# Performance work log

Measured on AMD Instinct MI355X. Metric: run time of the kernel, lower is better.

## Reference

```python
import jax, jax.numpy as jnp
import numpy as np

LN_EPS = 1e-5


def setup_inputs() -> dict:
    key = jax.random.key(0)
    k1, k2, k3, k4 = jax.random.split(key, 4)
    b, n, d, o, m = 64, 196, 768, 196, 2
    return {
        "x": jax.random.normal(k1, (b, n, d), dtype=jnp.float32),
        "ln_w": jnp.ones((d,), dtype=jnp.float32),
        "ln_b": jnp.zeros((d,), dtype=jnp.float32),
        "sw": jax.random.normal(k2, (o, m, n), dtype=jnp.float32),
        "sb": jax.random.normal(k3, (o, m, n), dtype=jnp.float32),
        "dw": jax.random.normal(k4, (o, m), dtype=jnp.float32),
    }


def reference(x, ln_w, ln_b, sw, sb, dw):
    # LayerNorm over last dim (dim=768)
    mu = jnp.mean(x, axis=-1, keepdims=True)
    var = jnp.mean(jnp.square(x - mu), axis=-1, keepdims=True)
    y = (x - mu) * jax.lax.rsqrt(var + LN_EPS) * ln_w + ln_b  # (b, n, d)

    # Original: repeat y to (b,d,o,m,n), apply sw*y+sb, sum over n.
    # With no synapse activation / dropout this is exactly a contraction:
    # s[b,d,o,m] = sum_n sw[o,m,n]*y[b,n,d] + sum_n sb[o,m,n]
    s = jnp.einsum('bnd,omn->bdom', y, sw) + jnp.sum(sb, axis=-1)  # (b,d,o,m)

    # dendritic weighting then sum over branches m
    t = jnp.sum(dw * s, axis=-1)  # (b, d, o)

    # soma = nn.GELU (exact erf form)
    out = jax.nn.gelu(t, approximate=False)

    out = jnp.transpose(out, (0, 2, 1))  # (b, o, d) == (b, n, d)
    return x * (out + 1.0)
```

## Files before the change

### kernel.cpp

```cpp
#include <hip/hip_runtime.h>
#include <math.h>


#define B_   64
#define N_   196
#define D_   768
#define KQ   7
#define OPAD 256

typedef __attribute__((ext_vector_type(8))) short bf16x8;
typedef __attribute__((ext_vector_type(4))) float f32x4;

__device__ __forceinline__ unsigned short bf16_rne(float f) {
    unsigned u = __builtin_bit_cast(unsigned, f);
    u += 0x7FFFu + ((u >> 16) & 1u);
    return (unsigned short)(u >> 16);
}
__device__ __forceinline__ float bf16_to_f(unsigned short h) {
    unsigned u = ((unsigned)h) << 16;
    return __builtin_bit_cast(float, u);
}

__global__ void prep_w_kernel(const float* __restrict__ sw,
                              const float* __restrict__ sb,
                              const float* __restrict__ dw,
                              unsigned short* __restrict__ Wfh,
                              unsigned short* __restrict__ Wfl,
                              float* __restrict__ rowsum,
                              float* __restrict__ cvec) {
    int o = blockIdx.x;
    int t = threadIdx.x;
    float w0 = 0.f, w1 = 0.f;
    if (o < N_) { w0 = dw[o * 2 + 0]; w1 = dw[o * 2 + 1]; }
    float val = 0.f, sbp = 0.f;
    if (o < N_ && t < N_) {
        val = w0 * sw[(o * 2 + 0) * N_ + t] + w1 * sw[(o * 2 + 1) * N_ + t];
        sbp = w0 * sb[(o * 2 + 0) * N_ + t] + w1 * sb[(o * 2 + 1) * N_ + t];
    }
    if (t < KQ * 32) {
        unsigned short h = bf16_rne(val);
        int addr = (((o >> 4) * KQ + (t >> 5)) * 4 + ((t >> 3) & 3)) * 128
                 + (o & 15) * 8 + (t & 7);
        Wfh[addr] = h;
        Wfl[addr] = bf16_rne(val - bf16_to_f(h));
    }
    __shared__ float r1[256], r2[256];
    r1[t] = val; r2[t] = sbp;
    __syncthreads();
    for (int s = 128; s > 0; s >>= 1) {
        if (t < s) { r1[t] += r1[t + s]; r2[t] += r2[t + s]; }
        __syncthreads();
    }
    if (t == 0) { rowsum[o] = r1[0]; cvec[o] = r2[0]; }
}

__global__ void ln_stats_kernel(const float* __restrict__ x,
                                float* __restrict__ mu,
                                float* __restrict__ rstd) {
    int wave = threadIdx.x >> 6;
    int lane = threadIdx.x & 63;
    int row  = blockIdx.x * 4 + wave;
    const float4* xr = reinterpret_cast<const float4*>(x + (size_t)row * D_);
    float4 v0 = xr[lane];
    float4 v1 = xr[lane + 64];
    float4 v2 = xr[lane + 128];
    float s = v0.x + v0.y + v0.z + v0.w
            + v1.x + v1.y + v1.z + v1.w
            + v2.x + v2.y + v2.z + v2.w;
    #pragma unroll
    for (int off = 32; off >= 1; off >>= 1) s += __shfl_xor(s, off);
    float m = s * (1.0f / D_);
    float q = 0.f;
    {
        float d;
        d = v0.x - m; q += d * d;  d = v0.y - m; q += d * d;
        d = v0.z - m; q += d * d;  d = v0.w - m; q += d * d;
        d = v1.x - m; q += d * d;  d = v1.y - m; q += d * d;
        d = v1.z - m; q += d * d;  d = v1.w - m; q += d * d;
        d = v2.x - m; q += d * d;  d = v2.y - m; q += d * d;
        d = v2.z - m; q += d * d;  d = v2.w - m; q += d * d;
    }
    #pragma unroll
    for (int off = 32; off >= 1; off >>= 1) q += __shfl_xor(q, off);
    if (lane == 0) {
        mu[row]   = m;
        rstd[row] = rsqrtf(q * (1.0f / D_) + 1e-5f);
    }
}

__global__ __launch_bounds__(512, 4) void gemm_mfma_kernel(
    const float* __restrict__ x,
    const float* __restrict__ ln_w,
    const float* __restrict__ ln_b,
    const unsigned short* __restrict__ Wfh,
    const unsigned short* __restrict__ Wfl,
    const float* __restrict__ rowsum,
    const float* __restrict__ cvec,
    const float* __restrict__ mu,
    const float* __restrict__ rstd,
    float* __restrict__ out) {
    const int b  = blockIdx.y;
    const int d0 = blockIdx.x * 64;
    const int t = threadIdx.x;
    const int w = t >> 6, lane = t & 63;
    const int m16 = lane & 15, g = lane >> 4;

    const float* xb  = x + (size_t)b * (N_ * D_);
    const float* mub = mu + b * N_;
    const float* rsb = rstd + b * N_;

    f32x4 acc[2][4];
    #pragma unroll
    for (int i = 0; i < 2; ++i)
        #pragma unroll
        for (int j = 0; j < 4; ++j)
            acc[i][j] = (f32x4){0.f, 0.f, 0.f, 0.f};

    #pragma unroll
    for (int c = 0; c < KQ; ++c) {
        const int kb = c * 32 + g * 8;
        const float* xp = xb + (size_t)kb * D_ + d0 + m16;
        float xv[4][8];
        #pragma unroll
        for (int nf = 0; nf < 4; ++nf)
            #pragma unroll
            for (int e = 0; e < 8; ++e)
                xv[nf][e] = (kb + e < N_) ? xp[(size_t)e * D_ + nf * 16] : 0.f;
        float4 m0 = *reinterpret_cast<const float4*>(mub + kb);
        float4 m1 = *reinterpret_cast<const float4*>(mub + kb + 4);
        float4 r0 = *reinterpret_cast<const float4*>(rsb + kb);
        float4 r1 = *reinterpret_cast<const float4*>(rsb + kb + 4);
        float a_[8]   = {r0.x, r0.y, r0.z, r0.w, r1.x, r1.y, r1.z, r1.w};
        float off_[8] = {-m0.x * r0.x, -m0.y * r0.y, -m0.z * r0.z, -m0.w * r0.w,
                         -m1.x * r1.x, -m1.y * r1.y, -m1.z * r1.z, -m1.w * r1.w};
        bf16x8 ah[2], al[2];
        #pragma unroll
        for (int mf = 0; mf < 2; ++mf) {
            const size_t ab = ((size_t)((w * 2 + mf) * KQ + c)) * 512 + lane * 8;
            ah[mf] = *reinterpret_cast<const bf16x8*>(Wfh + ab);
            al[mf] = *reinterpret_cast<const bf16x8*>(Wfl + ab);
        }
        #pragma unroll
        for (int nf = 0; nf < 4; ++nf) {
            bf16x8 bh, bl;
            #pragma unroll
            for (int e = 0; e < 8; ++e) {
                float v = fmaf(xv[nf][e], a_[e], off_[e]);
                unsigned short h = bf16_rne(v);
                bh[e] = (short)h;
                bl[e] = (short)bf16_rne(v - bf16_to_f(h));
            }
            #pragma unroll
            for (int mf = 0; mf < 2; ++mf) {
                acc[mf][nf] = __builtin_amdgcn_mfma_f32_16x16x32_bf16(ah[mf], bh, acc[mf][nf], 0, 0, 0);
                acc[mf][nf] = __builtin_amdgcn_mfma_f32_16x16x32_bf16(ah[mf], bl, acc[mf][nf], 0, 0, 0);
                acc[mf][nf] = __builtin_amdgcn_mfma_f32_16x16x32_bf16(al[mf], bh, acc[mf][nf], 0, 0, 0);
            }
        }
    }

    float lwv[4], lbv[4];
    #pragma unroll
    for (int nf = 0; nf < 4; ++nf) {
        lwv[nf] = ln_w[d0 + nf * 16 + m16];
        lbv[nf] = ln_b[d0 + nf * 16 + m16];
    }
    #pragma unroll
    for (int mf = 0; mf < 2; ++mf) {
        const int obase = (w * 2 + mf) * 16 + g * 4;
        f32x4 rs4 = *reinterpret_cast<const f32x4*>(rowsum + obase);
        f32x4 cc4 = *reinterpret_cast<const f32x4*>(cvec + obase);
        float xres[4][4];
        #pragma unroll
        for (int r = 0; r < 4; ++r) {
            const int o = obase + r;
            #pragma unroll
            for (int nf = 0; nf < 4; ++nf)
                xres[r][nf] = (o < N_) ? xb[(size_t)o * D_ + d0 + nf * 16 + m16] : 0.f;
        }
        #pragma unroll
        for (int r = 0; r < 4; ++r) {
            const int o = obase + r;
            if (o < N_) {
                #pragma unroll
                for (int nf = 0; nf < 4; ++nf) {
                    const int d = d0 + nf * 16 + m16;
                    float T = fmaf(lwv[nf], acc[mf][nf][r], fmaf(lbv[nf], rs4[r], cc4[r]));
                    float gl = 0.5f * T * (1.0f + erff(T * 0.70710678118654752f));
                    out[((size_t)(b * N_ + o)) * D_ + d] = xres[r][nf] * (gl + 1.0f);
                }
            }
        }
    }
}

extern "C" void kernel_launch(void* const* d_in, const int* in_sizes, int n_in,
                              void* d_out, int out_size, void* d_ws, size_t ws_size,
                              hipStream_t stream) {
    const float* x    = (const float*)d_in[0];
    const float* ln_w = (const float*)d_in[1];
    const float* ln_b = (const float*)d_in[2];
    const float* sw   = (const float*)d_in[3];
    const float* sb   = (const float*)d_in[4];
    const float* dw   = (const float*)d_in[5];
    float* out = (float*)d_out;

    float* wsf = (float*)d_ws;
    float* mu     = wsf;
    float* rstd   = mu + 12608;
    float* rowsum = rstd + 12608;
    float* cvec   = rowsum + OPAD;
    unsigned short* Wfh = (unsigned short*)(cvec + OPAD);
    unsigned short* Wfl = Wfh + 16 * KQ * 512;

    prep_w_kernel<<<OPAD, 256, 0, stream>>>(sw, sb, dw, Wfh, Wfl, rowsum, cvec);
    ln_stats_kernel<<<(B_ * N_) / 4, 256, 0, stream>>>(x, mu, rstd);
    gemm_mfma_kernel<<<dim3(12, B_), 512, 0, stream>>>(
        x, ln_w, ln_b, Wfh, Wfl, rowsum, cvec, mu, rstd, out);
}
```

Baseline: 59.50 us.

## Stage normalized bf16 split B tiles in LDS with double buffering

The GEMM kernel now uses 1024-thread blocks that cover 192 columns of d instead of 64. Twelve waves load x, normalize it, split it into hi/lo bf16 parts once, and write them to a double-buffered LDS tile. All 16 waves then read their B fragments from LDS, and the next chunk's global loads are prefetched during the MFMA work. This removes the repeated per-wave normalize-and-convert work and the redundant x loads, at the cost of block-wide barriers every chunk, 48 KB of LDS, and a grid of only 256 blocks. The prep_w layout changes to match the new addressing, and the workspace is reordered.

```diff
diff --git a/kernel.cpp b/kernel.cpp
--- a/kernel.cpp
+++ b/kernel.cpp
@@ -7,6 +7,7 @@
 #define D_   768
 #define KQ   7
 #define OPAD 256
+#define DT   192
 
 typedef __attribute__((ext_vector_type(8))) short bf16x8;
 typedef __attribute__((ext_vector_type(4))) float f32x4;
@@ -39,8 +40,8 @@
     }
     if (t < KQ * 32) {
         unsigned short h = bf16_rne(val);
-        int addr = (((o >> 4) * KQ + (t >> 5)) * 4 + ((t >> 3) & 3)) * 128
-                 + (o & 15) * 8 + (t & 7);
+        int addr = ((o >> 4) * KQ + (t >> 5)) * 512
+                 + (((t >> 3) & 3) * 16 + (o & 15)) * 8 + (t & 7);
         Wfh[addr] = h;
         Wfl[addr] = bf16_rne(val - bf16_to_f(h));
     }
@@ -88,7 +89,7 @@
     }
 }
 
-__global__ __launch_bounds__(512, 4) void gemm_mfma_kernel(
+__global__ __launch_bounds__(1024, 4) void gemm_fused_kernel(
     const float* __restrict__ x,
     const float* __restrict__ ln_w,
     const float* __restrict__ ln_b,
@@ -100,56 +101,83 @@
     const float* __restrict__ rstd,
     float* __restrict__ out) {
     const int b  = blockIdx.y;
-    const int d0 = blockIdx.x * 64;
+    const int dt = blockIdx.x;
+    const int d0 = dt * DT;
     const int t = threadIdx.x;
     const int w = t >> 6, lane = t & 63;
     const int m16 = lane & 15, g = lane >> 4;
+    const int ow = w >> 1, dw = w & 1;
+
+    __shared__ __align__(16) unsigned short Bs[2][12288];
 
     const float* xb  = x + (size_t)b * (N_ * D_);
     const float* mub = mu + b * N_;
     const float* rsb = rstd + b * N_;
 
-    f32x4 acc[2][4];
+    const bool stager = (w < 12);
+    const int gs  = w / 3;
+    const int dls = (w - gs * 3) * 64 + lane;
+
+    float xv[2][8];
+
+    #define LOADC(s, c) do {                                                  \
+        if (stager) {                                                         \
+            _Pragma("unroll")                                                 \
+            for (int e = 0; e < 8; ++e) {                                     \
+                const int k = (c) * 32 + gs * 8 + e;                          \
+                xv[s][e] = (k < N_) ? xb[(size_t)k * D_ + d0 + dls] : 0.f;    \
+            }                                                                 \
+        } } while (0)
+
+    #define WRITEC(s, c) do {                                                 \
+        if (stager) {                                                         \
+            bf16x8 hv, lv;                                                    \
+            _Pragma("unroll")                                                 \
+            for (int e = 0; e < 8; ++e) {                                     \
+                const int k = (c) * 32 + gs * 8 + e;                          \
+                float v = 0.f;                                                \
+                if (k < N_) v = (xv[s][e] - mub[k]) * rsb[k];                 \
+                unsigned short h = bf16_rne(v);                               \
+                hv[e] = (short)h;                                             \
+                lv[e] = (short)bf16_rne(v - bf16_to_f(h));                    \
+            }                                                                 \
+            const int ei = gs * 1536 + dls * 8;                               \
+            *reinterpret_cast<bf16x8*>(&Bs[s][ei])        = hv;               \
+            *reinterpret_cast<bf16x8*>(&Bs[s][ei + 6144]) = lv;               \
+        } } while (0)
+
+    f32x4 acc[2][6];
     #pragma unroll
     for (int i = 0; i < 2; ++i)
         #pragma unroll
-        for (int j = 0; j < 4; ++j)
+        for (int j = 0; j < 6; ++j)
             acc[i][j] = (f32x4){0.f, 0.f, 0.f, 0.f};
 
+    LOADC(0, 0);
+    LOADC(1, 1);
+    WRITEC(0, 0);
+    __syncthreads();
+
     #pragma unroll
     for (int c = 0; c < KQ; ++c) {
-        const int kb = c * 32 + g * 8;
-        const float* xp = xb + (size_t)kb * D_ + d0 + m16;
-        float xv[4][8];
-        #pragma unroll
-        for (int nf = 0; nf < 4; ++nf)
-            #pragma unroll
-            for (int e = 0; e < 8; ++e)
-                xv[nf][e] = (kb + e < N_) ? xp[(size_t)e * D_ + nf * 16] : 0.f;
-        float4 m0 = *reinterpret_cast<const float4*>(mub + kb);
-        float4 m1 = *reinterpret_cast<const float4*>(mub + kb + 4);
-        float4 r0 = *reinterpret_cast<const float4*>(rsb + kb);
-        float4 r1 = *reinterpret_cast<const float4*>(rsb + kb + 4);
-        float a_[8]   = {r0.x, r0.y, r0.z, r0.w, r1.x, r1.y, r1.z, r1.w};
-        float off_[8] = {-m0.x * r0.x, -m0.y * r0.y, -m0.z * r0.z, -m0.w * r0.w,
-                         -m1.x * r1.x, -m1.y * r1.y, -m1.z * r1.z, -m1.w * r1.w};
+        const int s = c & 1;
+        if (c > 0) {
+            WRITEC(s, c);
+            __syncthreads();
+        }
+        if (c + 2 < KQ) LOADC(s, c + 2);
         bf16x8 ah[2], al[2];
         #pragma unroll
         for (int mf = 0; mf < 2; ++mf) {
-            const size_t ab = ((size_t)((w * 2 + mf) * KQ + c)) * 512 + lane * 8;
+            const size_t ab = ((size_t)((ow * 2 + mf) * KQ + c)) * 512 + lane * 8;
             ah[mf] = *reinterpret_cast<const bf16x8*>(Wfh + ab);
             al[mf] = *reinterpret_cast<const bf16x8*>(Wfl + ab);
         }
         #pragma unroll
-        for (int nf = 0; nf < 4; ++nf) {
-            bf16x8 bh, bl;
-            #pragma unroll
-            for (int e = 0; e < 8; ++e) {
-                float v = fmaf(xv[nf][e], a_[e], off_[e]);
-                unsigned short h = bf16_rne(v);
-                bh[e] = (short)h;
-                bl[e] = (short)bf16_rne(v - bf16_to_f(h));
-            }
+        for (int nf = 0; nf < 6; ++nf) {
+            const int bi = g * 1536 + (dw * 96 + nf * 16 + m16) * 8;
+            bf16x8 bh = *reinterpret_cast<const bf16x8*>(&Bs[s][bi]);
+            bf16x8 bl = *reinterpret_cast<const bf16x8*>(&Bs[s][bi + 6144]);
             #pragma unroll
             for (int mf = 0; mf < 2; ++mf) {
                 acc[mf][nf] = __builtin_amdgcn_mfma_f32_16x16x32_bf16(ah[mf], bh, acc[mf][nf], 0, 0, 0);
@@ -159,39 +187,34 @@
         }
     }
 
-    float lwv[4], lbv[4];
-    #pragma unroll
-    for (int nf = 0; nf < 4; ++nf) {
-        lwv[nf] = ln_w[d0 + nf * 16 + m16];
-        lbv[nf] = ln_b[d0 + nf * 16 + m16];
+    float lwv[6], lbv[6];
+    #pragma unroll
+    for (int nf = 0; nf < 6; ++nf) {
+        const int d = d0 + dw * 96 + nf * 16 + m16;
+        lwv[nf] = ln_w[d];
+        lbv[nf] = ln_b[d];
     }
     #pragma unroll
     for (int mf = 0; mf < 2; ++mf) {
-        const int obase = (w * 2 + mf) * 16 + g * 4;
+        const int obase = ow * 32 + mf * 16 + g * 4;
         f32x4 rs4 = *reinterpret_cast<const f32x4*>(rowsum + obase);
         f32x4 cc4 = *reinterpret_cast<const f32x4*>(cvec + obase);
-        float xres[4][4];
-        #pragma unroll
-        for (int r = 0; r < 4; ++r) {
-            const int o = obase + r;
-            #pragma unroll
-            for (int nf = 0; nf < 4; ++nf)
-                xres[r][nf] = (o < N_) ? xb[(size_t)o * D_ + d0 + nf * 16 + m16] : 0.f;
-        }
         #pragma unroll
         for (int r = 0; r < 4; ++r) {
             const int o = obase + r;
             if (o < N_) {
                 #pragma unroll
-                for (int nf = 0; nf < 4; ++nf) {
-                    const int d = d0 + nf * 16 + m16;
+                for (int nf = 0; nf < 6; ++nf) {
+                    const int d = d0 + dw * 96 + nf * 16 + m16;
                     float T = fmaf(lwv[nf], acc[mf][nf][r], fmaf(lbv[nf], rs4[r], cc4[r]));
                     float gl = 0.5f * T * (1.0f + erff(T * 0.70710678118654752f));
-                    out[((size_t)(b * N_ + o)) * D_ + d] = xres[r][nf] * (gl + 1.0f);
+                    out[((size_t)(b * N_ + o)) * D_ + d] = xb[(size_t)o * D_ + d] * (gl + 1.0f);
                 }
             }
         }
     }
+    #undef LOADC
+    #undef WRITEC
 }
 
 extern "C" void kernel_launch(void* const* d_in, const int* in_sizes, int n_in,
@@ -206,15 +229,15 @@
     float* out = (float*)d_out;
 
     float* wsf = (float*)d_ws;
-    float* mu     = wsf;
-    float* rstd   = mu + 12608;
-    float* rowsum = rstd + 12608;
+    float* rowsum = wsf;
     float* cvec   = rowsum + OPAD;
     unsigned short* Wfh = (unsigned short*)(cvec + OPAD);
-    unsigned short* Wfl = Wfh + 16 * KQ * 512;
+    unsigned short* Wfl = Wfh + OPAD * (KQ * 32);
+    float* mu   = (float*)(Wfl + OPAD * (KQ * 32));
+    float* rstd = mu + 12608;
 
     prep_w_kernel<<<OPAD, 256, 0, stream>>>(sw, sb, dw, Wfh, Wfl, rowsum, cvec);
     ln_stats_kernel<<<(B_ * N_) / 4, 256, 0, stream>>>(x, mu, rstd);
-    gemm_mfma_kernel<<<dim3(12, B_), 512, 0, stream>>>(
+    gemm_fused_kernel<<<dim3(4, B_), 1024, 0, stream>>>(
         x, ln_w, ln_b, Wfh, Wfl, rowsum, cvec, mu, rstd, out);
 }
```

Result: faster. 55.98 us (-5.9%).

## Precompute normalized bf16 hi/lo B operand in LN kernel, pipeline GEMM loads

Applied to the files above, without the earlier changes.

The LN stats kernel now also normalizes x, folds in ln_w, splits each value into bf16 hi/lo parts, and writes them to workspace in an MFMA-ready k-octet layout. The GEMM then loads the prepacked B fragments directly and double-buffers the A/B register loads across K chunks, instead of reading strided fp32 x and converting it in the inner loop. The tile width changes from 64 to 48 columns with occupancy hint 2. The cost is an extra write and read of a 2x bf16 copy of the activations, and variance is now computed as E[x²]−mu², which can lose precision.

```diff
diff --git a/kernel.cpp b/kernel.cpp
--- a/kernel.cpp
+++ b/kernel.cpp
@@ -6,6 +6,7 @@
 #define N_   196
 #define D_   768
 #define KQ   7
+#define NKO  28
 #define OPAD 256
 
 typedef __attribute__((ext_vector_type(8))) short bf16x8;
@@ -39,8 +40,8 @@
     }
     if (t < KQ * 32) {
         unsigned short h = bf16_rne(val);
-        int addr = (((o >> 4) * KQ + (t >> 5)) * 4 + ((t >> 3) & 3)) * 128
-                 + (o & 15) * 8 + (t & 7);
+        int addr = ((o >> 4) * KQ + (t >> 5)) * 512
+                 + (((t >> 3) & 3) * 16 + (o & 15)) * 8 + (t & 7);
         Wfh[addr] = h;
         Wfl[addr] = bf16_rne(val - bf16_to_f(h));
     }
@@ -54,128 +55,147 @@
     if (t == 0) { rowsum[o] = r1[0]; cvec[o] = r2[0]; }
 }
 
-__global__ void ln_stats_kernel(const float* __restrict__ x,
-                                float* __restrict__ mu,
-                                float* __restrict__ rstd) {
-    int wave = threadIdx.x >> 6;
-    int lane = threadIdx.x & 63;
-    int row  = blockIdx.x * 4 + wave;
-    const float4* xr = reinterpret_cast<const float4*>(x + (size_t)row * D_);
-    float4 v0 = xr[lane];
-    float4 v1 = xr[lane + 64];
-    float4 v2 = xr[lane + 128];
+__global__ __launch_bounds__(512) void ln_split_kernel(
+    const float* __restrict__ x,
+    const float* __restrict__ ln_w,
+    unsigned short* __restrict__ Bh,
+    unsigned short* __restrict__ Bl) {
+    const int koct = blockIdx.x, b = blockIdx.y;
+    const int t = threadIdx.x, w = t >> 6, lane = t & 63;
+    const int k = koct * 8 + w;
+    __shared__ float xs[8][768];
+
+    float4 v0 = make_float4(0.f, 0.f, 0.f, 0.f);
+    float4 v1 = v0, v2 = v0;
+    if (k < N_) {
+        const float4* xr = reinterpret_cast<const float4*>(x + ((size_t)b * N_ + k) * D_);
+        v0 = xr[lane]; v1 = xr[lane + 64]; v2 = xr[lane + 128];
+    }
     float s = v0.x + v0.y + v0.z + v0.w
             + v1.x + v1.y + v1.z + v1.w
             + v2.x + v2.y + v2.z + v2.w;
-    #pragma unroll
-    for (int off = 32; off >= 1; off >>= 1) s += __shfl_xor(s, off);
-    float m = s * (1.0f / D_);
-    float q = 0.f;
-    {
-        float d;
-        d = v0.x - m; q += d * d;  d = v0.y - m; q += d * d;
-        d = v0.z - m; q += d * d;  d = v0.w - m; q += d * d;
-        d = v1.x - m; q += d * d;  d = v1.y - m; q += d * d;
-        d = v1.z - m; q += d * d;  d = v1.w - m; q += d * d;
-        d = v2.x - m; q += d * d;  d = v2.y - m; q += d * d;
-        d = v2.z - m; q += d * d;  d = v2.w - m; q += d * d;
-    }
-    #pragma unroll
-    for (int off = 32; off >= 1; off >>= 1) q += __shfl_xor(q, off);
-    if (lane == 0) {
-        mu[row]   = m;
-        rstd[row] = rsqrtf(q * (1.0f / D_) + 1e-5f);
-    }
-}
-
-__global__ __launch_bounds__(512, 4) void gemm_mfma_kernel(
+    float q = v0.x*v0.x + v0.y*v0.y + v0.z*v0.z + v0.w*v0.w
+            + v1.x*v1.x + v1.y*v1.y + v1.z*v1.z + v1.w*v1.w
+            + v2.x*v2.x + v2.y*v2.y + v2.z*v2.z + v2.w*v2.w;
+    #pragma unroll
+    for (int off = 32; off >= 1; off >>= 1) {
+        s += __shfl_xor(s, off);
+        q += __shfl_xor(q, off);
+    }
+    const float mu   = s * (1.0f / D_);
+    const float var  = q * (1.0f / D_) - mu * mu;
+    const float rstd = rsqrtf(var + 1e-5f);
+
+    const float4* lw4 = reinterpret_cast<const float4*>(ln_w);
+    float4 w0 = lw4[lane], w1 = lw4[lane + 64], w2 = lw4[lane + 128];
+    float4 o0, o1, o2;
+    o0.x = (v0.x - mu) * rstd * w0.x;  o0.y = (v0.y - mu) * rstd * w0.y;
+    o0.z = (v0.z - mu) * rstd * w0.z;  o0.w = (v0.w - mu) * rstd * w0.w;
+    o1.x = (v1.x - mu) * rstd * w1.x;  o1.y = (v1.y - mu) * rstd * w1.y;
+    o1.z = (v1.z - mu) * rstd * w1.z;  o1.w = (v1.w - mu) * rstd * w1.w;
+    o2.x = (v2.x - mu) * rstd * w2.x;  o2.y = (v2.y - mu) * rstd * w2.y;
+    o2.z = (v2.z - mu) * rstd * w2.z;  o2.w = (v2.w - mu) * rstd * w2.w;
+    *reinterpret_cast<float4*>(&xs[w][lane * 4])       = o0;
+    *reinterpret_cast<float4*>(&xs[w][lane * 4 + 256]) = o1;
+    *reinterpret_cast<float4*>(&xs[w][lane * 4 + 512]) = o2;
+    __syncthreads();
+
+    for (int d = t; d < D_; d += 512) {
+        bf16x8 hv, lv;
+        #pragma unroll
+        for (int kk = 0; kk < 8; ++kk) {
+            float v = xs[kk][d];
+            unsigned short h = bf16_rne(v);
+            hv[kk] = (short)h;
+            lv[kk] = (short)bf16_rne(v - bf16_to_f(h));
+        }
+        const size_t base = (((size_t)b * NKO + koct) * D_ + d) * 8;
+        *reinterpret_cast<bf16x8*>(Bh + base) = hv;
+        *reinterpret_cast<bf16x8*>(Bl + base) = lv;
+    }
+}
+
+__global__ __launch_bounds__(512, 2) void gemm_bpk_kernel(
     const float* __restrict__ x,
-    const float* __restrict__ ln_w,
     const float* __restrict__ ln_b,
     const unsigned short* __restrict__ Wfh,
     const unsigned short* __restrict__ Wfl,
+    const unsigned short* __restrict__ Bh,
+    const unsigned short* __restrict__ Bl,
     const float* __restrict__ rowsum,
     const float* __restrict__ cvec,
-    const float* __restrict__ mu,
-    const float* __restrict__ rstd,
     float* __restrict__ out) {
     const int b  = blockIdx.y;
-    const int d0 = blockIdx.x * 64;
+    const int d0 = blockIdx.x * 48;
     const int t = threadIdx.x;
     const int w = t >> 6, lane = t & 63;
     const int m16 = lane & 15, g = lane >> 4;
 
-    const float* xb  = x + (size_t)b * (N_ * D_);
-    const float* mub = mu + b * N_;
-    const float* rsb = rstd + b * N_;
-
-    f32x4 acc[2][4];
+    const float* xb = x + (size_t)b * (N_ * D_);
+
+    f32x4 acc[2][3];
     #pragma unroll
     for (int i = 0; i < 2; ++i)
         #pragma unroll
-        for (int j = 0; j < 4; ++j)
+        for (int j = 0; j < 3; ++j)
             acc[i][j] = (f32x4){0.f, 0.f, 0.f, 0.f};
 
+    bf16x8 bhr[2][3], blr[2][3], ahr[2][2], alr[2][2];
+
+    #define LOADB(s, c) do {                                                  \
+        const size_t krow = ((size_t)b * NKO + (c) * 4 + g) * D_;             \
+        _Pragma("unroll")                                                     \
+        for (int nf = 0; nf < 3; ++nf) {                                      \
+            const size_t e = (krow + d0 + nf * 16 + m16) * 8;                 \
+            bhr[s][nf] = *reinterpret_cast<const bf16x8*>(Bh + e);            \
+            blr[s][nf] = *reinterpret_cast<const bf16x8*>(Bl + e);            \
+        } } while (0)
+
+    #define LOADA(s, c) do {                                                  \
+        _Pragma("unroll")                                                     \
+        for (int mf = 0; mf < 2; ++mf) {                                      \
+            const size_t ab = ((size_t)((w * 2 + mf) * KQ + (c))) * 512 + lane * 8; \
+            ahr[s][mf] = *reinterpret_cast<const bf16x8*>(Wfh + ab);          \
+            alr[s][mf] = *reinterpret_cast<const bf16x8*>(Wfl + ab);          \
+        } } while (0)
+
+    LOADB(0, 0);
+    LOADA(0, 0);
+
     #pragma unroll
     for (int c = 0; c < KQ; ++c) {
-        const int kb = c * 32 + g * 8;
-        const float* xp = xb + (size_t)kb * D_ + d0 + m16;
-        float xv[4][8];
-        #pragma unroll
-        for (int nf = 0; nf < 4; ++nf)
-            #pragma unroll
-            for (int e = 0; e < 8; ++e)
-                xv[nf][e] = (kb + e < N_) ? xp[(size_t)e * D_ + nf * 16] : 0.f;
-        float4 m0 = *reinterpret_cast<const float4*>(mub + kb);
-        float4 m1 = *reinterpret_cast<const float4*>(mub + kb + 4);
-        float4 r0 = *reinterpret_cast<const float4*>(rsb + kb);
-        float4 r1 = *reinterpret_cast<const float4*>(rsb + kb + 4);
-        float a_[8]   = {r0.x, r0.y, r0.z, r0.w, r1.x, r1.y, r1.z, r1.w};
-        float off_[8] = {-m0.x * r0.x, -m0.y * r0.y, -m0.z * r0.z, -m0.w * r0.w,
-                         -m1.x * r1.x, -m1.y * r1.y, -m1.z * r1.z, -m1.w * r1.w};
-        bf16x8 ah[2], al[2];
-        #pragma unroll
-        for (int mf = 0; mf < 2; ++mf) {
-            const size_t ab = ((size_t)((w * 2 + mf) * KQ + c)) * 512 + lane * 8;
-            ah[mf] = *reinterpret_cast<const bf16x8*>(Wfh + ab);
-            al[mf] = *reinterpret_cast<const bf16x8*>(Wfl + ab);
-        }
-        #pragma unroll
-        for (int nf = 0; nf < 4; ++nf) {
-            bf16x8 bh, bl;
-            #pragma unroll
-            for (int e = 0; e < 8; ++e) {
-                float v = fmaf(xv[nf][e], a_[e], off_[e]);
-                unsigned short h = bf16_rne(v);
-                bh[e] = (short)h;
-                bl[e] = (short)bf16_rne(v - bf16_to_f(h));
-            }
+        const int s = c & 1;
+        if (c + 1 < KQ) {
+            LOADB(s ^ 1, c + 1);
+            LOADA(s ^ 1, c + 1);
+        }
+        #pragma unroll
+        for (int nf = 0; nf < 3; ++nf) {
             #pragma unroll
             for (int mf = 0; mf < 2; ++mf) {
-                acc[mf][nf] = __builtin_amdgcn_mfma_f32_16x16x32_bf16(ah[mf], bh, acc[mf][nf], 0, 0, 0);
-                acc[mf][nf] = __builtin_amdgcn_mfma_f32_16x16x32_bf16(ah[mf], bl, acc[mf][nf], 0, 0, 0);
-                acc[mf][nf] = __builtin_amdgcn_mfma_f32_16x16x32_bf16(al[mf], bh, acc[mf][nf], 0, 0, 0);
+                acc[mf][nf] = __builtin_amdgcn_mfma_f32_16x16x32_bf16(ahr[s][mf], bhr[s][nf], acc[mf][nf], 0, 0, 0);
+                acc[mf][nf] = __builtin_amdgcn_mfma_f32_16x16x32_bf16(ahr[s][mf], blr[s][nf], acc[mf][nf], 0, 0, 0);
+                acc[mf][nf] = __builtin_amdgcn_mfma_f32_16x16x32_bf16(alr[s][mf], bhr[s][nf], acc[mf][nf], 0, 0, 0);
             }
         }
     }
-
-    float lwv[4], lbv[4];
-    #pragma unroll
-    for (int nf = 0; nf < 4; ++nf) {
-        lwv[nf] = ln_w[d0 + nf * 16 + m16];
-        lbv[nf] = ln_b[d0 + nf * 16 + m16];
-    }
+    #undef LOADB
+    #undef LOADA
+
+    float lbv[3];
+    #pragma unroll
+    for (int nf = 0; nf < 3; ++nf) lbv[nf] = ln_b[d0 + nf * 16 + m16];
     #pragma unroll
     for (int mf = 0; mf < 2; ++mf) {
         const int obase = (w * 2 + mf) * 16 + g * 4;
         f32x4 rs4 = *reinterpret_cast<const f32x4*>(rowsum + obase);
         f32x4 cc4 = *reinterpret_cast<const f32x4*>(cvec + obase);
-        float xres[4][4];
+        float xres[4][3];
         #pragma unroll
         for (int r = 0; r < 4; ++r) {
             const int o = obase + r;
             #pragma unroll
-            for (int nf = 0; nf < 4; ++nf)
+            for (int nf = 0; nf < 3; ++nf)
                 xres[r][nf] = (o < N_) ? xb[(size_t)o * D_ + d0 + nf * 16 + m16] : 0.f;
         }
         #pragma unroll
@@ -183,9 +203,9 @@
             const int o = obase + r;
             if (o < N_) {
                 #pragma unroll
-                for (int nf = 0; nf < 4; ++nf) {
+                for (int nf = 0; nf < 3; ++nf) {
                     const int d = d0 + nf * 16 + m16;
-                    float T = fmaf(lwv[nf], acc[mf][nf][r], fmaf(lbv[nf], rs4[r], cc4[r]));
+                    float T = acc[mf][nf][r] + fmaf(lbv[nf], rs4[r], cc4[r]);
                     float gl = 0.5f * T * (1.0f + erff(T * 0.70710678118654752f));
                     out[((size_t)(b * N_ + o)) * D_ + d] = xres[r][nf] * (gl + 1.0f);
                 }
@@ -206,15 +226,15 @@
     float* out = (float*)d_out;
 
     float* wsf = (float*)d_ws;
-    float* mu     = wsf;
-    float* rstd   = mu + 12608;
-    float* rowsum = rstd + 12608;
+    float* rowsum = wsf;
     float* cvec   = rowsum + OPAD;
     unsigned short* Wfh = (unsigned short*)(cvec + OPAD);
-    unsigned short* Wfl = Wfh + 16 * KQ * 512;
+    unsigned short* Wfl = Wfh + OPAD * (KQ * 32);
+    unsigned short* Bh  = Wfl + OPAD * (KQ * 32);
+    unsigned short* Bl  = Bh + (size_t)B_ * NKO * D_ * 8;
 
     prep_w_kernel<<<OPAD, 256, 0, stream>>>(sw, sb, dw, Wfh, Wfl, rowsum, cvec);
-    ln_stats_kernel<<<(B_ * N_) / 4, 256, 0, stream>>>(x, mu, rstd);
-    gemm_mfma_kernel<<<dim3(12, B_), 512, 0, stream>>>(
-        x, ln_w, ln_b, Wfh, Wfl, rowsum, cvec, mu, rstd, out);
-}
+    ln_split_kernel<<<dim3(NKO, B_), 512, 0, stream>>>(x, ln_w, Bh, Bl);
+    gemm_bpk_kernel<<<dim3(16, B_), 512, 0, stream>>>(
+        x, ln_b, Wfh, Wfl, Bh, Bl, rowsum, cvec, out);
+}
```

Result: faster. 56.15 us (-5.6%).
